# Optimization experiments

Measured on AMD Instinct MI355X. Metric: run time of the kernel, lower is better.

Reference implementation:

```python
import jax, jax.numpy as jnp
import numpy as np

EPS = 1e-08


def _similarity_transform(S1, S2):
    """Batched Procrustes: S1, S2 are [B, 3, N]. Returns aligned S1_hat [B, 3, N]."""
    mu1 = jnp.mean(S1, axis=-1, keepdims=True)          # [B,3,1]
    mu2 = jnp.mean(S2, axis=-1, keepdims=True)
    X1 = S1 - mu1
    X2 = S2 - mu2
    var1 = jnp.sum(X1 * X1, axis=(1, 2))                # [B]
    # cross-covariance K = X1 @ X2^T + eps (eps added to every entry, as in torch ref)
    K = jnp.einsum('bin,bjn->bij', X1, X2) + EPS        # [B,3,3]
    U, s, Vh = jnp.linalg.svd(K, full_matrices=False)
    V = jnp.swapaxes(Vh, -1, -2)
    # det(U @ V^T) = det(U @ Vh); sign has zero gradient, same as torch
    sign = jax.lax.stop_gradient(jnp.sign(jnp.linalg.det(jnp.matmul(U, Vh))))  # [B]
    ones = jnp.ones_like(sign)
    d = jnp.stack([ones, ones, sign], axis=-1)          # diag of Z, [B,3]
    # R = V @ Z @ U^T
    R = jnp.einsum('bik,bk,bjk->bij', V, d, U)          # [B,3,3]
    scale = jnp.einsum('bij,bji->b', R, K) / var1       # trace(R@K)/var1, [B]
    t = mu2 - scale[:, None, None] * jnp.matmul(R, mu1)  # [B,3,1]
    S1_hat = scale[:, None, None] * jnp.matmul(R, S1) + t
    return S1_hat


def setup_inputs() -> dict:
    key = jax.random.key(0)
    k1, k2 = jax.random.split(key)
    B, N = 1024, 6890
    pred = jax.random.normal(k1, (B, N, 3), dtype=jnp.float32)
    gt = jax.random.normal(k2, (B, N, 3), dtype=jnp.float32)
    return {"pred": pred, "gt": gt}


def reference(pred, gt):
    # inputs are [B, N, 3] -> torch code transposes to [B, 3, N] and back
    S1 = jnp.swapaxes(pred, 1, 2)
    S2 = jnp.swapaxes(gt, 1, 2)
    S1_hat = jnp.swapaxes(_similarity_transform(S1, S2), 1, 2)  # [B,N,3]
    # loss_type == 'l1', reduction='none'
    return jnp.abs(S1_hat - gt)
```

## Files before the change

kernel.cpp:

```cpp
#include <hip/hip_runtime.h>
#include <math.h>

#define NPTS 6890
#define BATCH 1024

__global__ __launch_bounds__(256) void reduce_kernel(
    const float* __restrict__ pred, const float* __restrict__ gt,
    float* __restrict__ sums) {
  const int b = blockIdx.x;
  const float* __restrict__ p = pred + (size_t)b * (NPTS * 3);
  const float* __restrict__ g = gt   + (size_t)b * (NPTS * 3);

  float acc[16];
#pragma unroll
  for (int i = 0; i < 16; ++i) acc[i] = 0.f;

  for (int n = threadIdx.x; n < NPTS; n += 256) {
    const int j = 3 * n;
    const float p0 = p[j], p1 = p[j + 1], p2 = p[j + 2];
    const float g0 = g[j], g1 = g[j + 1], g2 = g[j + 2];
    acc[0] += p0;  acc[1] += p1;  acc[2] += p2;
    acc[3] += g0;  acc[4] += g1;  acc[5] += g2;
    acc[6] += p0 * p0 + p1 * p1 + p2 * p2;
    acc[7]  += p0 * g0;  acc[8]  += p0 * g1;  acc[9]  += p0 * g2;
    acc[10] += p1 * g0;  acc[11] += p1 * g1;  acc[12] += p1 * g2;
    acc[13] += p2 * g0;  acc[14] += p2 * g1;  acc[15] += p2 * g2;
  }

#pragma unroll
  for (int i = 0; i < 16; ++i) {
#pragma unroll
    for (int off = 32; off > 0; off >>= 1)
      acc[i] += __shfl_down(acc[i], off, 64);
  }

  __shared__ float red[4][16];
  const int wave = threadIdx.x >> 6;
  const int lane = threadIdx.x & 63;
  if (lane == 0) {
#pragma unroll
    for (int i = 0; i < 16; ++i) red[wave][i] = acc[i];
  }
  __syncthreads();
  if (threadIdx.x < 16) {
    const int i = threadIdx.x;
    sums[b * 16 + i] = red[0][i] + red[1][i] + red[2][i] + red[3][i];
  }
}

__global__ void solve_kernel(const float* __restrict__ sums,
                             float* __restrict__ params) {
  const int b = blockIdx.x * blockDim.x + threadIdx.x;
  if (b >= BATCH) return;
  const float* s = sums + b * 16;
  const double Ninv = 1.0 / (double)NPTS;

  double sp[3] = {s[0], s[1], s[2]};
  double sg[3] = {s[3], s[4], s[5]};
  double mu1[3], mu2[3];
#pragma unroll
  for (int i = 0; i < 3; ++i) { mu1[i] = sp[i] * Ninv; mu2[i] = sg[i] * Ninv; }
  const double var1 =
      (double)s[6] - (sp[0] * sp[0] + sp[1] * sp[1] + sp[2] * sp[2]) * Ninv;

  double K[3][3];
#pragma unroll
  for (int i = 0; i < 3; ++i)
#pragma unroll
    for (int j = 0; j < 3; ++j)
      K[i][j] = (double)s[7 + 3 * i + j] - sp[i] * sg[j] * Ninv + 1e-8;

  double A[3][3];
#pragma unroll
  for (int i = 0; i < 3; ++i)
#pragma unroll
    for (int j = 0; j < 3; ++j)
      A[i][j] = K[0][i] * K[0][j] + K[1][i] * K[1][j] + K[2][i] * K[2][j];

  double V[3][3] = {{1, 0, 0}, {0, 1, 0}, {0, 0, 1}};
  for (int sweep = 0; sweep < 30; ++sweep) {
    const double off = A[0][1] * A[0][1] + A[0][2] * A[0][2] + A[1][2] * A[1][2];
    const double nrm = A[0][0] + A[1][1] + A[2][2];
    if (off <= 1e-30 * nrm * nrm) break;
    for (int pq = 0; pq < 3; ++pq) {
      const int p = (pq == 2) ? 1 : 0;
      const int q = (pq == 0) ? 1 : 2;
      const double apq = A[p][q];
      if (apq == 0.0) continue;
      const double theta = (A[q][q] - A[p][p]) / (2.0 * apq);
      const double tt =
          ((theta >= 0.0) ? 1.0 : -1.0) / (fabs(theta) + sqrt(theta * theta + 1.0));
      const double c = 1.0 / sqrt(tt * tt + 1.0);
      const double sn = tt * c;
      const double app = A[p][p], aqq = A[q][q];
      A[p][p] = app - tt * apq;
      A[q][q] = aqq + tt * apq;
      A[p][q] = 0.0; A[q][p] = 0.0;
      const int r = 3 - p - q;
      const double arp = A[r][p], arq = A[r][q];
      A[r][p] = c * arp - sn * arq; A[p][r] = A[r][p];
      A[r][q] = sn * arp + c * arq; A[q][r] = A[r][q];
#pragma unroll
      for (int k = 0; k < 3; ++k) {
        const double vkp = V[k][p], vkq = V[k][q];
        V[k][p] = c * vkp - sn * vkq;
        V[k][q] = sn * vkp + c * vkq;
      }
    }
  }

  double w[3] = {A[0][0], A[1][1], A[2][2]};
  int i0 = 0, i1 = 1, i2 = 2, tmp;
  if (w[i0] < w[i1]) { tmp = i0; i0 = i1; i1 = tmp; }
  if (w[i0] < w[i2]) { tmp = i0; i0 = i2; i2 = tmp; }
  if (w[i1] < w[i2]) { tmp = i1; i1 = i2; i2 = tmp; }
  const double sv0 = sqrt(fmax(w[i0], 0.0));
  const double sv1 = sqrt(fmax(w[i1], 0.0));
  const double sv2 = sqrt(fmax(w[i2], 0.0));

  const double detK =
      K[0][0] * (K[1][1] * K[2][2] - K[1][2] * K[2][1]) -
      K[0][1] * (K[1][0] * K[2][2] - K[1][2] * K[2][0]) +
      K[0][2] * (K[1][0] * K[2][1] - K[1][1] * K[2][0]);
  const double sgn = (detK > 0.0) ? 1.0 : ((detK < 0.0) ? -1.0 : 0.0);

  const double floor0 = sv0 * 1e-12 + 1e-300;
  const double z0 = 1.0 / fmax(sv0, floor0);
  const double z1 = 1.0 / fmax(sv1, floor0);
  const double z2 = sgn / fmax(sv2, floor0);

  double W[3][3];
#pragma unroll
  for (int a = 0; a < 3; ++a)
#pragma unroll
    for (int c = 0; c < 3; ++c)
      W[a][c] = V[a][i0] * V[c][i0] * z0 + V[a][i1] * V[c][i1] * z1 +
                V[a][i2] * V[c][i2] * z2;

  double R[3][3];
#pragma unroll
  for (int a = 0; a < 3; ++a)
#pragma unroll
    for (int c = 0; c < 3; ++c)
      R[a][c] = W[a][0] * K[c][0] + W[a][1] * K[c][1] + W[a][2] * K[c][2];

  const double trace = sv0 + sv1 + sgn * sv2;
  const double scale = trace / var1;

  float* pr = params + b * 12;
#pragma unroll
  for (int a = 0; a < 3; ++a) {
#pragma unroll
    for (int c = 0; c < 3; ++c) pr[3 * a + c] = (float)(scale * R[a][c]);
    pr[9 + a] = (float)(mu2[a] - scale * (R[a][0] * mu1[0] + R[a][1] * mu1[1] +
                                          R[a][2] * mu1[2]));
  }
}

__global__ __launch_bounds__(256) void apply_kernel(
    const float* __restrict__ pred, const float* __restrict__ gt,
    const float* __restrict__ params, float* __restrict__ out) {
  const int b = blockIdx.y;
  const int n = blockIdx.x * blockDim.x + threadIdx.x;
  const float* pr = params + b * 12;
  const float m00 = pr[0], m01 = pr[1], m02 = pr[2];
  const float m10 = pr[3], m11 = pr[4], m12 = pr[5];
  const float m20 = pr[6], m21 = pr[7], m22 = pr[8];
  const float t0 = pr[9], t1 = pr[10], t2 = pr[11];
  if (n < NPTS) {
    const size_t base = ((size_t)b * NPTS + n) * 3;
    const float p0 = pred[base], p1 = pred[base + 1], p2 = pred[base + 2];
    const float g0 = gt[base], g1 = gt[base + 1], g2 = gt[base + 2];
    out[base]     = fabsf(m00 * p0 + m01 * p1 + m02 * p2 + t0 - g0);
    out[base + 1] = fabsf(m10 * p0 + m11 * p1 + m12 * p2 + t1 - g1);
    out[base + 2] = fabsf(m20 * p0 + m21 * p1 + m22 * p2 + t2 - g2);
  }
}

extern "C" void kernel_launch(void* const* d_in, const int* in_sizes, int n_in,
                              void* d_out, int out_size, void* d_ws, size_t ws_size,
                              hipStream_t stream) {
  const float* pred = (const float*)d_in[0];
  const float* gt   = (const float*)d_in[1];
  float* out = (float*)d_out;
  float* sums   = (float*)d_ws;
  float* params = sums + BATCH * 16;

  hipLaunchKernelGGL(reduce_kernel, dim3(BATCH), dim3(256), 0, stream,
                     pred, gt, sums);
  hipLaunchKernelGGL(solve_kernel, dim3((BATCH + 255) / 256), dim3(256), 0,
                     stream, sums, params);
  hipLaunchKernelGGL(apply_kernel, dim3((NPTS + 255) / 256, BATCH), dim3(256),
                     0, stream, pred, gt, params, out);
}
```

Baseline: 248.5 us.

## Vectorize reduce and apply kernels with aligned float4 loads over point groups

Both the reduction and apply kernels now process groups of four points as three float4 loads and stores per tensor instead of scalar strided accesses. Odd batches start two points in so the vector base is 16-byte aligned, and the two leftover points per batch are handled by a scalar tail. This cuts the number of memory instructions and should improve coalescing on a bandwidth-bound workload. The cost is more complex indexing and a tail path, and it relies on specific alignment of the batch offsets.

```diff
diff --git a/kernel.cpp b/kernel.cpp
--- a/kernel.cpp
+++ b/kernel.cpp
@@ -3,28 +3,47 @@
 
 #define NPTS 6890
 #define BATCH 1024
+#define FLOATS_PER_BATCH (NPTS * 3)
+#define NGROUPS 1722
+
+__device__ __forceinline__ void accum(float* acc, float p0, float p1, float p2,
+                                      float g0, float g1, float g2) {
+  acc[0] += p0;  acc[1] += p1;  acc[2] += p2;
+  acc[3] += g0;  acc[4] += g1;  acc[5] += g2;
+  acc[6] += p0 * p0 + p1 * p1 + p2 * p2;
+  acc[7]  += p0 * g0;  acc[8]  += p0 * g1;  acc[9]  += p0 * g2;
+  acc[10] += p1 * g0;  acc[11] += p1 * g1;  acc[12] += p1 * g2;
+  acc[13] += p2 * g0;  acc[14] += p2 * g1;  acc[15] += p2 * g2;
+}
 
 __global__ __launch_bounds__(256) void reduce_kernel(
     const float* __restrict__ pred, const float* __restrict__ gt,
     float* __restrict__ sums) {
   const int b = blockIdx.x;
-  const float* __restrict__ p = pred + (size_t)b * (NPTS * 3);
-  const float* __restrict__ g = gt   + (size_t)b * (NPTS * 3);
+  const size_t ofs0 = (size_t)b * FLOATS_PER_BATCH;
+  const int skip = (b & 1) ? 2 : 0;
+  const size_t ofs = ofs0 + (size_t)skip * 3;
+  const float4* __restrict__ p4 = (const float4*)(pred + ofs);
+  const float4* __restrict__ g4 = (const float4*)(gt + ofs);
 
   float acc[16];
 #pragma unroll
   for (int i = 0; i < 16; ++i) acc[i] = 0.f;
 
-  for (int n = threadIdx.x; n < NPTS; n += 256) {
-    const int j = 3 * n;
-    const float p0 = p[j], p1 = p[j + 1], p2 = p[j + 2];
-    const float g0 = g[j], g1 = g[j + 1], g2 = g[j + 2];
-    acc[0] += p0;  acc[1] += p1;  acc[2] += p2;
-    acc[3] += g0;  acc[4] += g1;  acc[5] += g2;
-    acc[6] += p0 * p0 + p1 * p1 + p2 * p2;
-    acc[7]  += p0 * g0;  acc[8]  += p0 * g1;  acc[9]  += p0 * g2;
-    acc[10] += p1 * g0;  acc[11] += p1 * g1;  acc[12] += p1 * g2;
-    acc[13] += p2 * g0;  acc[14] += p2 * g1;  acc[15] += p2 * g2;
+  for (int gi = threadIdx.x; gi < NGROUPS; gi += 256) {
+    const float4 a0 = p4[3 * gi], a1 = p4[3 * gi + 1], a2 = p4[3 * gi + 2];
+    const float4 c0 = g4[3 * gi], c1 = g4[3 * gi + 1], c2 = g4[3 * gi + 2];
+    accum(acc, a0.x, a0.y, a0.z, c0.x, c0.y, c0.z);
+    accum(acc, a0.w, a1.x, a1.y, c0.w, c1.x, c1.y);
+    accum(acc, a1.z, a1.w, a2.x, c1.z, c1.w, c2.x);
+    accum(acc, a2.y, a2.z, a2.w, c2.y, c2.z, c2.w);
+  }
+
+  if (threadIdx.x < 2) {
+    const int n = skip ? (int)threadIdx.x : (NPTS - 2 + (int)threadIdx.x);
+    const float* pp = pred + ofs0 + 3 * n;
+    const float* gg = gt + ofs0 + 3 * n;
+    accum(acc, pp[0], pp[1], pp[2], gg[0], gg[1], gg[2]);
   }
 
 #pragma unroll
@@ -157,23 +176,47 @@
   }
 }
 
+__device__ __forceinline__ void xform(const float* m, float p0, float p1,
+                                      float p2, float g0, float g1, float g2,
+                                      float& o0, float& o1, float& o2) {
+  o0 = fabsf(m[0] * p0 + m[1] * p1 + m[2] * p2 + m[9] - g0);
+  o1 = fabsf(m[3] * p0 + m[4] * p1 + m[5] * p2 + m[10] - g1);
+  o2 = fabsf(m[6] * p0 + m[7] * p1 + m[8] * p2 + m[11] - g2);
+}
+
 __global__ __launch_bounds__(256) void apply_kernel(
     const float* __restrict__ pred, const float* __restrict__ gt,
     const float* __restrict__ params, float* __restrict__ out) {
   const int b = blockIdx.y;
-  const int n = blockIdx.x * blockDim.x + threadIdx.x;
-  const float* pr = params + b * 12;
-  const float m00 = pr[0], m01 = pr[1], m02 = pr[2];
-  const float m10 = pr[3], m11 = pr[4], m12 = pr[5];
-  const float m20 = pr[6], m21 = pr[7], m22 = pr[8];
-  const float t0 = pr[9], t1 = pr[10], t2 = pr[11];
-  if (n < NPTS) {
-    const size_t base = ((size_t)b * NPTS + n) * 3;
-    const float p0 = pred[base], p1 = pred[base + 1], p2 = pred[base + 2];
-    const float g0 = gt[base], g1 = gt[base + 1], g2 = gt[base + 2];
-    out[base]     = fabsf(m00 * p0 + m01 * p1 + m02 * p2 + t0 - g0);
-    out[base + 1] = fabsf(m10 * p0 + m11 * p1 + m12 * p2 + t1 - g1);
-    out[base + 2] = fabsf(m20 * p0 + m21 * p1 + m22 * p2 + t2 - g2);
+  float m[12];
+#pragma unroll
+  for (int i = 0; i < 12; ++i) m[i] = params[b * 12 + i];
+
+  const size_t ofs0 = (size_t)b * FLOATS_PER_BATCH;
+  const int skip = (b & 1) ? 2 : 0;
+  const size_t ofs = ofs0 + (size_t)skip * 3;
+  const int gi = blockIdx.x * 256 + threadIdx.x;
+
+  if (gi < NGROUPS) {
+    const float4* __restrict__ p4 = (const float4*)(pred + ofs);
+    const float4* __restrict__ g4 = (const float4*)(gt + ofs);
+    float4* __restrict__ o4 = (float4*)(out + ofs);
+    const float4 a0 = p4[3 * gi], a1 = p4[3 * gi + 1], a2 = p4[3 * gi + 2];
+    const float4 c0 = g4[3 * gi], c1 = g4[3 * gi + 1], c2 = g4[3 * gi + 2];
+    float4 r0, r1, r2;
+    xform(m, a0.x, a0.y, a0.z, c0.x, c0.y, c0.z, r0.x, r0.y, r0.z);
+    xform(m, a0.w, a1.x, a1.y, c0.w, c1.x, c1.y, r0.w, r1.x, r1.y);
+    xform(m, a1.z, a1.w, a2.x, c1.z, c1.w, c2.x, r1.z, r1.w, r2.x);
+    xform(m, a2.y, a2.z, a2.w, c2.y, c2.z, c2.w, r2.y, r2.z, r2.w);
+    o4[3 * gi] = r0; o4[3 * gi + 1] = r1; o4[3 * gi + 2] = r2;
+  }
+
+  if (blockIdx.x == 0 && threadIdx.x < 2) {
+    const int n = skip ? (int)threadIdx.x : (NPTS - 2 + (int)threadIdx.x);
+    const float* pp = pred + ofs0 + 3 * n;
+    const float* gg = gt + ofs0 + 3 * n;
+    float* oo = out + ofs0 + 3 * n;
+    xform(m, pp[0], pp[1], pp[2], gg[0], gg[1], gg[2], oo[0], oo[1], oo[2]);
   }
 }
 
@@ -190,6 +233,6 @@
                      pred, gt, sums);
   hipLaunchKernelGGL(solve_kernel, dim3((BATCH + 255) / 256), dim3(256), 0,
                      stream, sums, params);
-  hipLaunchKernelGGL(apply_kernel, dim3((NPTS + 255) / 256, BATCH), dim3(256),
-                     0, stream, pred, gt, params, out);
-}
+  hipLaunchKernelGGL(apply_kernel, dim3((NGROUPS + 255) / 256, BATCH),
+                     dim3(256), 0, stream, pred, gt, params, out);
+}
```

Result: no change. 246.3 us (-0.9%).
